# Kernel tuning notes

Measured on AMD Instinct MI355X. Metric: run time of the kernel, lower is better.

## Reference

```python
import jax, jax.numpy as jnp
import numpy as np

NUM_EMBEDDINGS = 8192
EMBEDDING_DIM = 512
BATCH = 32768
COMMITMENT_COST = 0.25
DECAY = 0.99


def setup_inputs() -> dict:
    key = jax.random.key(0)
    k1, k2, k3 = jax.random.split(key, 3)
    z = jax.random.normal(k1, (BATCH, EMBEDDING_DIM), dtype=jnp.float32)
    # codebook initialized uniform(-1/K, 1/K) as in the torch module
    codebook = jax.random.uniform(k2, (NUM_EMBEDDINGS, EMBEDDING_DIM), dtype=jnp.float32,
                                  minval=-1.0 / NUM_EMBEDDINGS, maxval=1.0 / NUM_EMBEDDINGS)
    ema_cluster_size = jnp.zeros((NUM_EMBEDDINGS,), dtype=jnp.float32)
    ema_embedding_sum = codebook.copy()
    return {"z": z, "codebook": codebook, "ema_cluster_size": ema_cluster_size,
            "ema_embedding_sum": ema_embedding_sum}


def reference(z, codebook, ema_cluster_size, ema_embedding_sum):
    K, D = codebook.shape
    B = z.shape[0]
    # squared-euclidean distances: ||z||^2 - 2 z W^T + ||W||^2  -> [B, K]
    distances = (jnp.sum(z * z, axis=1, keepdims=True)
                 - 2.0 * jnp.einsum('bd,kd->bk', z, codebook)
                 + jnp.sum(codebook * codebook, axis=1)[None, :])
    indices = jnp.argmin(distances, axis=1)            # [B]
    quantized = codebook[indices]                      # [B, D] gather

    commitment_loss = jnp.mean((z - jax.lax.stop_gradient(quantized)) ** 2)
    codebook_loss = jnp.mean((quantized - jax.lax.stop_gradient(z)) ** 2)
    vq_loss = codebook_loss + COMMITMENT_COST * commitment_loss

    # EMA statistics (training-mode buffer update, no grad)
    cluster_size = jax.ops.segment_sum(jnp.ones((B,), jnp.float32), indices, num_segments=K)
    embedding_sum = jax.ops.segment_sum(z, indices, num_segments=K)  # one-hot^T @ z
    new_ema_cluster_size = DECAY * ema_cluster_size + (1.0 - DECAY) * cluster_size
    new_ema_embedding_sum = DECAY * ema_embedding_sum + (1.0 - DECAY) * embedding_sum
    n = jnp.sum(new_ema_cluster_size)
    cs_norm = (new_ema_cluster_size + 1e-5) / (n + K * 1e-5) * n
    new_codebook = new_ema_embedding_sum / cs_norm[:, None]

    # straight-through estimator
    quantized_st = z + jax.lax.stop_gradient(quantized - z)

    # perplexity of code usage
    avg_probs = cluster_size / B
    perplexity = jnp.exp(-jnp.sum(avg_probs * jnp.log(avg_probs + 1e-10)))

    return (quantized_st, indices, commitment_loss, codebook_loss, vq_loss,
            perplexity, new_ema_cluster_size, new_ema_embedding_sum, new_codebook)
```

## Files before the change

### kernel.cpp

```cpp
#include <hip/hip_runtime.h>
#include <math.h>

typedef unsigned long long u64;
typedef unsigned int u32;
typedef unsigned short u16;
typedef __attribute__((ext_vector_type(8))) short bf16x8;
typedef __attribute__((ext_vector_type(8))) u16  u16x8;
typedef __attribute__((ext_vector_type(4))) float f32x4;

#define KC 8192
#define DD 512
#define BB 32768
#define NSPLIT 4
#define KRANGE (KC / NSPLIT)
#define BMM 128
#define BNN 128
#define NCT (KRANGE / BNN)
#define TOPS 4

#define WS_SEG   0ull
#define WS_CNT   (WS_SEG + (size_t)KC * DD * 4)
#define WS_LOSS  (WS_CNT + (size_t)KC * 4)
#define WS_W2    (WS_LOSS + 8)
#define WS_ZZ    (WS_W2 + (size_t)KC * 4)
#define WS_TI    (WS_ZZ + (size_t)BB * 4)
#define WS_CSN   (WS_TI + (size_t)NSPLIT * BB * TOPS * 4)
#define WS_WB    (WS_CSN + (size_t)KC * 4)
#define ZERO_BYTES (WS_LOSS + 8)

#define OQ  0ull
#define OI  ((size_t)BB * DD)
#define OS  (OI + BB)
#define ONC (OS + 4)
#define ONS (ONC + KC)
#define OCB (ONS + (size_t)KC * DD)

__device__ __forceinline__ u64 sortable_pack(float e, int col) {
    u32 s = __float_as_uint(e);
    s = (s & 0x80000000u) ? ~s : (s | 0x80000000u);
    return ((u64)s << 32) | (u32)col;
}
__device__ __forceinline__ u64 umin64(u64 a, u64 b) { return a < b ? a : b; }
__device__ __forceinline__ u64 umax64(u64 a, u64 b) { return a > b ? a : b; }
__device__ __forceinline__ u16 f2bf(float f) {
    u32 u = __float_as_uint(f);
    u32 r = u + 0x7FFFu + ((u >> 16) & 1u);
    return (u16)(r >> 16);
}

__global__ __launch_bounds__(256)
void cvt_kernel(const float* __restrict__ in, u16* __restrict__ out, int n8) {
    int i = blockIdx.x * 256 + threadIdx.x;
    if (i >= n8) return;
    float4 a = ((const float4*)in)[2 * i];
    float4 b = ((const float4*)in)[2 * i + 1];
    u16x8 r = { f2bf(a.x), f2bf(a.y), f2bf(a.z), f2bf(a.w),
                f2bf(b.x), f2bf(b.y), f2bf(b.z), f2bf(b.w) };
    ((u16x8*)out)[i] = r;
}

__global__ __launch_bounds__(256)
void np_sqnorm_kernel(const float* __restrict__ in, float* __restrict__ out, int rows) {
    int r = blockIdx.x * 256 + threadIdx.x;
    if (r >= rows) return;
    const float* p = in + (size_t)r * DD;
    float Bv[4];
#pragma unroll
    for (int blk = 0; blk < 4; blk++) {
        const float4* p4 = (const float4*)(p + blk * 128);
        float4 a = p4[0], b = p4[1];
        float a0 = __fmul_rn(a.x, a.x), a1 = __fmul_rn(a.y, a.y);
        float a2 = __fmul_rn(a.z, a.z), a3 = __fmul_rn(a.w, a.w);
        float a4 = __fmul_rn(b.x, b.x), a5 = __fmul_rn(b.y, b.y);
        float a6 = __fmul_rn(b.z, b.z), a7 = __fmul_rn(b.w, b.w);
#pragma unroll
        for (int t = 1; t < 16; t++) {
            a = p4[2 * t]; b = p4[2 * t + 1];
            a0 = __fadd_rn(a0, __fmul_rn(a.x, a.x)); a1 = __fadd_rn(a1, __fmul_rn(a.y, a.y));
            a2 = __fadd_rn(a2, __fmul_rn(a.z, a.z)); a3 = __fadd_rn(a3, __fmul_rn(a.w, a.w));
            a4 = __fadd_rn(a4, __fmul_rn(b.x, b.x)); a5 = __fadd_rn(a5, __fmul_rn(b.y, b.y));
            a6 = __fadd_rn(a6, __fmul_rn(b.z, b.z)); a7 = __fadd_rn(a7, __fmul_rn(b.w, b.w));
        }
        Bv[blk] = __fadd_rn(__fadd_rn(__fadd_rn(a0, a1), __fadd_rn(a2, a3)),
                            __fadd_rn(__fadd_rn(a4, a5), __fadd_rn(a6, a7)));
    }
    out[r] = __fadd_rn(__fadd_rn(Bv[0], Bv[1]), __fadd_rn(Bv[2], Bv[3]));
}

__global__ __launch_bounds__(256, 2)
void pass1_mfma_kernel(const u16* __restrict__ Zb, const u16* __restrict__ Wb,
                       const float* __restrict__ w2, int* __restrict__ ti) {
    __shared__ u64 smem64[4224];
    char* smem = (char*)smem64;

    int bx = blockIdx.x;
    int bxs = (bx & 7) * 128 + (bx >> 3);
    int sp = bxs & 3;
    int rb = bxs >> 2;
    int row0 = rb * BMM, col0 = sp * KRANGE;

    int tid = threadIdx.x;
    int lane = tid & 63, wid = tid >> 6;
    int wr = wid >> 1, wc = wid & 1;
    int l15 = lane & 15, g = lane >> 4, l7 = lane & 7;
    int srow = lane >> 3;
    int schunk = l7 ^ srow;

    u64 K3[16][3];
#pragma unroll
    for (int s = 0; s < 16; s++) { K3[s][0] = ~0ull; K3[s][1] = ~0ull; K3[s][2] = ~0ull; }

    for (int ct = 0; ct < NCT; ++ct) {
        int kc0 = col0 + ct * BNN;
        f32x4 acc[4][4];
#pragma unroll
        for (int m = 0; m < 4; m++)
#pragma unroll
            for (int n = 0; n < 4; n++) acc[m][n] = (f32x4)(0.0f);

        for (int d0 = 0; d0 < DD; d0 += 64) {
            __syncthreads();
#pragma unroll
            for (int ii = 0; ii < 4; ii++) {
                int issue = wid * 4 + ii;
                int trow = issue * 8 + srow;
                const char* gpA = (const char*)Zb +
                    (((size_t)(row0 + trow) * DD) + d0 + schunk * 8) * 2;
                __builtin_amdgcn_global_load_lds((const void*)gpA,
                    (void*)(smem + issue * 1024), 16, 0, 0);
                const char* gpB = (const char*)Wb +
                    (((size_t)(kc0 + trow) * DD) + d0 + schunk * 8) * 2;
                __builtin_amdgcn_global_load_lds((const void*)gpB,
                    (void*)(smem + 16384 + issue * 1024), 16, 0, 0);
            }
            __syncthreads();
#pragma unroll
            for (int ks = 0; ks < 2; ks++) {
                int sA = ((ks * 4 + g) ^ l7) << 4;
                bf16x8 aF[4], bF[4];
#pragma unroll
                for (int m = 0; m < 4; m++) {
                    int ar = wr * 64 + m * 16 + l15;
                    aF[m] = *(const bf16x8*)(smem + ar * 128 + sA);
                }
#pragma unroll
                for (int n = 0; n < 4; n++) {
                    int br = wc * 64 + n * 16 + l15;
                    bF[n] = *(const bf16x8*)(smem + 16384 + br * 128 + sA);
                }
#pragma unroll
                for (int m = 0; m < 4; m++)
#pragma unroll
                    for (int n = 0; n < 4; n++)
                        acc[m][n] = __builtin_amdgcn_mfma_f32_16x16x32_bf16(
                            aF[m], bF[n], acc[m][n], 0, 0, 0);
            }
        }
#pragma unroll
        for (int n = 0; n < 4; n++) {
            int col = kc0 + wc * 64 + n * 16 + l15;
            float w2c = w2[col];
#pragma unroll
            for (int m = 0; m < 4; m++) {
#pragma unroll
                for (int r = 0; r < 4; r++) {
                    float e = fmaf(-2.0f, acc[m][n][r], w2c);
                    u64 x = sortable_pack(e, col);
                    int s = m * 4 + r;
                    if (x < K3[s][2]) {
                        u64 t1 = umax64(K3[s][0], x); K3[s][0] = umin64(K3[s][0], x);
                        u64 t2 = umax64(K3[s][1], t1); K3[s][1] = umin64(K3[s][1], t1);
                        K3[s][2] = umin64(K3[s][2], t2);
                    }
                }
            }
        }
    }

    u64* mb = smem64;
    for (int ph = 0; ph < 4; ph++) {
        __syncthreads();
        if (wr == (ph >> 1)) {
            int m0 = (ph & 1) * 2;
#pragma unroll
            for (int mi = 0; mi < 2; mi++) {
#pragma unroll
                for (int r = 0; r < 4; r++) {
                    int rip = mi * 16 + g * 4 + r;
                    int slot = wc * 16 + l15;
                    int s = (m0 + mi) * 4 + r;
                    u64* dst = &mb[rip * 97 + slot * 3];
                    dst[0] = K3[s][0]; dst[1] = K3[s][1]; dst[2] = K3[s][2];
                }
            }
        }
        __syncthreads();
        if (tid < 32) {
            u64 k0 = ~0ull, k1 = ~0ull, k2 = ~0ull, k3 = ~0ull;
            for (int e2 = 0; e2 < 96; e2++) {
                u64 x = mb[tid * 97 + e2];
                if (x < k3) {
                    u64 t1 = umax64(k0, x); k0 = umin64(k0, x);
                    u64 t2 = umax64(k1, t1); k1 = umin64(k1, t1);
                    u64 t3 = umax64(k2, t2); k2 = umin64(k2, t2);
                    k3 = umin64(k3, t3);
                }
            }
            int row = row0 + ph * 32 + tid;
            size_t o = ((size_t)sp * BB + row) * TOPS;
            ti[o + 0] = (int)(u32)k0;
            ti[o + 1] = (int)(u32)k1;
            ti[o + 2] = (int)(u32)k2;
            ti[o + 3] = (int)(u32)k3;
        }
    }
}

__global__ __launch_bounds__(256)
void rerank_kernel(const float* __restrict__ Z, const float* __restrict__ W,
                   const int* __restrict__ ti, const float* __restrict__ zzv,
                   const float* __restrict__ w2,
                   float* __restrict__ outq, float* __restrict__ outi,
                   float* __restrict__ counts, float* __restrict__ seg,
                   double* __restrict__ loss_acc) {
    int row = (blockIdx.x * blockDim.x + threadIdx.x) >> 6;
    int lane = threadIdx.x & 63;
    if (row >= BB) return;
    const float* zp = Z + (size_t)row * DD;
    float zf[8];
#pragma unroll
    for (int j = 0; j < 8; j++) zf[j] = zp[lane + j * 64];
    float zz = zzv[row];

    u64 best = ~0ull;
    for (int c = 0; c < NSPLIT * TOPS; c++) {
        int ix = ti[((size_t)(c >> 2) * BB + row) * TOPS + (c & 3)];
        const float* wp = W + (size_t)ix * DD;
        double dot = 0.0;
#pragma unroll
        for (int j = 0; j < 8; j++)
            dot = fma((double)zf[j], (double)wp[lane + j * 64], dot);
#pragma unroll
        for (int o = 32; o; o >>= 1) dot += __shfl_down(dot, o, 64);
        float E = (float)dot;
        E = __shfl(E, 0, 64);
        float dist = __fadd_rn(__fadd_rn(zz, __fmul_rn(-2.0f, E)), w2[ix]);
        u64 x = sortable_pack(dist, ix);
        best = umin64(best, x);
    }
    int besti = (int)(u32)best;

    if (!lane) { outi[row] = (float)besti; atomicAdd(&counts[besti], 1.0f); }
    const float* wp = W + (size_t)besti * DD;
    double ls = 0.0;
#pragma unroll
    for (int j = 0; j < 8; j++) {
        float q = wp[lane + j * 64];
        outq[(size_t)row * DD + lane + j * 64] = __fadd_rn(zf[j], __fsub_rn(q, zf[j]));
        float d = __fsub_rn(zf[j], q);
        ls = fma((double)d, (double)d, ls);
        atomicAdd(&seg[(size_t)besti * DD + lane + j * 64], zf[j]);
    }
#pragma unroll
    for (int o = 32; o; o >>= 1) ls += __shfl_down(ls, o, 64);
    if (!lane) atomicAdd(loss_acc, ls);
}

__global__ void finalize_kernel(const float* __restrict__ ema_cs,
                                const float* __restrict__ counts,
                                const double* __restrict__ loss_acc,
                                float* __restrict__ out_ncs,
                                float* __restrict__ out_scal,
                                float* __restrict__ csnorm) {
    __shared__ double sn[256], sh[256];
    int tid = threadIdx.x;
    double nl = 0.0, hl = 0.0;
    for (int k = tid; k < KC; k += 256) {
        float c = counts[k];
        float ncs = 0.99f * ema_cs[k] + 0.01f * c;
        out_ncs[k] = ncs;
        nl += (double)ncs;
        double p = (double)c * (1.0 / (double)BB);
        hl += p * log(p + 1e-10);
    }
    sn[tid] = nl; sh[tid] = hl; __syncthreads();
    for (int s = 128; s; s >>= 1) {
        if (tid < s) { sn[tid] += sn[tid + s]; sh[tid] += sh[tid + s]; }
        __syncthreads();
    }
    if (!tid) {
        double L = loss_acc[0] * (1.0 / ((double)BB * DD));
        out_scal[0] = (float)L;
        out_scal[1] = (float)L;
        out_scal[2] = (float)(L + 0.25 * L);
        out_scal[3] = (float)exp(-sh[0]);
    }
    double n = sn[0];
    for (int k = tid; k < KC; k += 256) {
        double ncs = (double)out_ncs[k];
        csnorm[k] = (float)((ncs + 1e-5) / (n + (double)KC * 1e-5) * n);
    }
}

__global__ __launch_bounds__(256)
void ema_kernel(const float* __restrict__ ema_sum, const float* __restrict__ seg,
                const float* __restrict__ csnorm,
                float* __restrict__ out_ns, float* __restrict__ out_cb) {
    int i = blockIdx.x * 256 + threadIdx.x;
    if (i >= KC * DD / 4) return;
    int k = i >> 7;
    float4 es = ((const float4*)ema_sum)[i];
    float4 sg = ((const float4*)seg)[i];
    float4 ns;
    ns.x = 0.99f * es.x + 0.01f * sg.x;
    ns.y = 0.99f * es.y + 0.01f * sg.y;
    ns.z = 0.99f * es.z + 0.01f * sg.z;
    ns.w = 0.99f * es.w + 0.01f * sg.w;
    ((float4*)out_ns)[i] = ns;
    float cn = csnorm[k];
    float4 cb; cb.x = ns.x / cn; cb.y = ns.y / cn; cb.z = ns.z / cn; cb.w = ns.w / cn;
    ((float4*)out_cb)[i] = cb;
}

extern "C" void kernel_launch(void* const* d_in, const int* in_sizes, int n_in,
                              void* d_out, int out_size, void* d_ws, size_t ws_size,
                              hipStream_t stream) {
    (void)in_sizes; (void)n_in; (void)out_size; (void)ws_size;
    const float* Z       = (const float*)d_in[0];
    const float* W       = (const float*)d_in[1];
    const float* ema_cs  = (const float*)d_in[2];
    const float* ema_sum = (const float*)d_in[3];
    float* out = (float*)d_out;
    char* ws = (char*)d_ws;

    float*  seg  = (float*)(ws + WS_SEG);
    float*  cnt  = (float*)(ws + WS_CNT);
    double* loss = (double*)(ws + WS_LOSS);
    float*  w2   = (float*)(ws + WS_W2);
    float*  zz   = (float*)(ws + WS_ZZ);
    int*    ti   = (int*)(ws + WS_TI);
    float*  csn  = (float*)(ws + WS_CSN);
    u16*    Wb   = (u16*)(ws + WS_WB);
    u16*    Zb   = (u16*)(out + OQ);

    hipMemsetAsync(ws, 0, ZERO_BYTES, stream);
    np_sqnorm_kernel<<<KC / 256, 256, 0, stream>>>(W, w2, KC);
    np_sqnorm_kernel<<<BB / 256, 256, 0, stream>>>(Z, zz, BB);
    cvt_kernel<<<(BB * DD / 8) / 256, 256, 0, stream>>>(Z, Zb, BB * DD / 8);
    cvt_kernel<<<(KC * DD / 8) / 256, 256, 0, stream>>>(W, Wb, KC * DD / 8);
    pass1_mfma_kernel<<<(BB / BMM) * NSPLIT, 256, 0, stream>>>(Zb, Wb, w2, ti);
    rerank_kernel<<<BB / 4, 256, 0, stream>>>(Z, W, ti, zz, w2, out + OQ, out + OI, cnt, seg, loss);
    finalize_kernel<<<1, 256, 0, stream>>>(ema_cs, cnt, loss, out + ONC, out + OS, csn);
    ema_kernel<<<KC * DD / 4 / 256, 256, 0, stream>>>(ema_sum, seg, csn, out + ONS, out + OCB);
}
```

Baseline: 1.607 ms.

## Prune rerank candidates by approximate-distance margin and parallelize row norms

New measurement: 1.490 ms. -7.3%, faster.

```diff
diff --git a/kernel.cpp b/kernel.cpp
--- a/kernel.cpp
+++ b/kernel.cpp
@@ -17,6 +17,7 @@
 #define BNN 128
 #define NCT (KRANGE / BNN)
 #define TOPS 4
+#define MARGIN 6e-4f
 
 #define WS_SEG   0ull
 #define WS_CNT   (WS_SEG + (size_t)KC * DD * 4)
@@ -24,7 +25,7 @@
 #define WS_W2    (WS_LOSS + 8)
 #define WS_ZZ    (WS_W2 + (size_t)KC * 4)
 #define WS_TI    (WS_ZZ + (size_t)BB * 4)
-#define WS_CSN   (WS_TI + (size_t)NSPLIT * BB * TOPS * 4)
+#define WS_CSN   (WS_TI + (size_t)NSPLIT * BB * TOPS * 8)
 #define WS_WB    (WS_CSN + (size_t)KC * 4)
 #define ZERO_BYTES (WS_LOSS + 8)
 
@@ -39,6 +40,11 @@
     u32 s = __float_as_uint(e);
     s = (s & 0x80000000u) ? ~s : (s | 0x80000000u);
     return ((u64)s << 32) | (u32)col;
+}
+__device__ __forceinline__ float sortable_unpack_val(u64 x) {
+    u32 s = (u32)(x >> 32);
+    u32 u = (s & 0x80000000u) ? (s & 0x7fffffffu) : ~s;
+    return __uint_as_float(u);
 }
 __device__ __forceinline__ u64 umin64(u64 a, u64 b) { return a < b ? a : b; }
 __device__ __forceinline__ u64 umax64(u64 a, u64 b) { return a > b ? a : b; }
@@ -61,42 +67,33 @@
 
 __global__ __launch_bounds__(256)
 void np_sqnorm_kernel(const float* __restrict__ in, float* __restrict__ out, int rows) {
-    int r = blockIdx.x * 256 + threadIdx.x;
+    int wv = (blockIdx.x * 256 + threadIdx.x) >> 6;
+    int lane = threadIdx.x & 63;
+    int r = wv * 2 + (lane >> 5);
     if (r >= rows) return;
-    const float* p = in + (size_t)r * DD;
-    float Bv[4];
-#pragma unroll
-    for (int blk = 0; blk < 4; blk++) {
-        const float4* p4 = (const float4*)(p + blk * 128);
-        float4 a = p4[0], b = p4[1];
-        float a0 = __fmul_rn(a.x, a.x), a1 = __fmul_rn(a.y, a.y);
-        float a2 = __fmul_rn(a.z, a.z), a3 = __fmul_rn(a.w, a.w);
-        float a4 = __fmul_rn(b.x, b.x), a5 = __fmul_rn(b.y, b.y);
-        float a6 = __fmul_rn(b.z, b.z), a7 = __fmul_rn(b.w, b.w);
-#pragma unroll
-        for (int t = 1; t < 16; t++) {
-            a = p4[2 * t]; b = p4[2 * t + 1];
-            a0 = __fadd_rn(a0, __fmul_rn(a.x, a.x)); a1 = __fadd_rn(a1, __fmul_rn(a.y, a.y));
-            a2 = __fadd_rn(a2, __fmul_rn(a.z, a.z)); a3 = __fadd_rn(a3, __fmul_rn(a.w, a.w));
-            a4 = __fadd_rn(a4, __fmul_rn(b.x, b.x)); a5 = __fadd_rn(a5, __fmul_rn(b.y, b.y));
-            a6 = __fadd_rn(a6, __fmul_rn(b.z, b.z)); a7 = __fadd_rn(a7, __fmul_rn(b.w, b.w));
-        }
-        Bv[blk] = __fadd_rn(__fadd_rn(__fadd_rn(a0, a1), __fadd_rn(a2, a3)),
-                            __fadd_rn(__fadd_rn(a4, a5), __fadd_rn(a6, a7)));
-    }
-    out[r] = __fadd_rn(__fadd_rn(Bv[0], Bv[1]), __fadd_rn(Bv[2], Bv[3]));
+    int l = lane & 31, b = l >> 3, a = l & 7;
+    const float* p = in + (size_t)r * DD + b * 128 + a;
+    float s = 0.0f;
+#pragma unroll
+    for (int t = 0; t < 16; t++) { float v = p[t * 8]; s = __fadd_rn(s, __fmul_rn(v, v)); }
+    s = __fadd_rn(s, __shfl_xor(s, 1, 64));
+    s = __fadd_rn(s, __shfl_xor(s, 2, 64));
+    s = __fadd_rn(s, __shfl_xor(s, 4, 64));
+    s = __fadd_rn(s, __shfl_xor(s, 8, 64));
+    s = __fadd_rn(s, __shfl_xor(s, 16, 64));
+    if (l == 0) out[r] = s;
 }
 
 __global__ __launch_bounds__(256, 2)
 void pass1_mfma_kernel(const u16* __restrict__ Zb, const u16* __restrict__ Wb,
-                       const float* __restrict__ w2, int* __restrict__ ti) {
+                       const float* __restrict__ w2, u64* __restrict__ ti) {
     __shared__ u64 smem64[4224];
     char* smem = (char*)smem64;
 
     int bx = blockIdx.x;
-    int bxs = (bx & 7) * 128 + (bx >> 3);
-    int sp = bxs & 3;
-    int rb = bxs >> 2;
+    int xcd = bx & 7, slot = bx >> 3;
+    int sp = xcd >> 1;
+    int rb = (xcd & 1) * 128 + slot;
     int row0 = rb * BMM, col0 = sp * KRANGE;
 
     int tid = threadIdx.x;
@@ -187,9 +184,9 @@
 #pragma unroll
                 for (int r = 0; r < 4; r++) {
                     int rip = mi * 16 + g * 4 + r;
-                    int slot = wc * 16 + l15;
+                    int slot2 = wc * 16 + l15;
                     int s = (m0 + mi) * 4 + r;
-                    u64* dst = &mb[rip * 97 + slot * 3];
+                    u64* dst = &mb[rip * 97 + slot2 * 3];
                     dst[0] = K3[s][0]; dst[1] = K3[s][1]; dst[2] = K3[s][2];
                 }
             }
@@ -208,17 +205,14 @@
             }
             int row = row0 + ph * 32 + tid;
             size_t o = ((size_t)sp * BB + row) * TOPS;
-            ti[o + 0] = (int)(u32)k0;
-            ti[o + 1] = (int)(u32)k1;
-            ti[o + 2] = (int)(u32)k2;
-            ti[o + 3] = (int)(u32)k3;
+            ti[o + 0] = k0; ti[o + 1] = k1; ti[o + 2] = k2; ti[o + 3] = k3;
         }
     }
 }
 
 __global__ __launch_bounds__(256)
 void rerank_kernel(const float* __restrict__ Z, const float* __restrict__ W,
-                   const int* __restrict__ ti, const float* __restrict__ zzv,
+                   const u64* __restrict__ ti, const float* __restrict__ zzv,
                    const float* __restrict__ w2,
                    float* __restrict__ outq, float* __restrict__ outi,
                    float* __restrict__ counts, float* __restrict__ seg,
@@ -232,9 +226,21 @@
     for (int j = 0; j < 8; j++) zf[j] = zp[lane + j * 64];
     float zz = zzv[row];
 
+    u64 cand = 0;
+    if (lane < 16) cand = ti[((size_t)(lane >> 2) * BB + row) * TOPS + (lane & 3)];
+    float cv = sortable_unpack_val(cand);
+    u64 mn = (lane < 16) ? cand : ~0ull;
+#pragma unroll
+    for (int o = 32; o; o >>= 1) mn = umin64(mn, __shfl_xor(mn, o, 64));
+    float vminf = sortable_unpack_val(mn);
+    bool surv = (lane < 16) && (cv <= vminf + MARGIN);
+    unsigned long long mask = __ballot(surv);
+
     u64 best = ~0ull;
-    for (int c = 0; c < NSPLIT * TOPS; c++) {
-        int ix = ti[((size_t)(c >> 2) * BB + row) * TOPS + (c & 3)];
+    while (mask) {
+        int c = (int)(__ffsll((long long)mask) - 1); mask &= mask - 1;
+        u64 cu = __shfl(cand, c, 64);
+        int ix = (int)(u32)cu;
         const float* wp = W + (size_t)ix * DD;
         double dot = 0.0;
 #pragma unroll
@@ -245,8 +251,7 @@
         float E = (float)dot;
         E = __shfl(E, 0, 64);
         float dist = __fadd_rn(__fadd_rn(zz, __fmul_rn(-2.0f, E)), w2[ix]);
-        u64 x = sortable_pack(dist, ix);
-        best = umin64(best, x);
+        best = umin64(best, sortable_pack(dist, ix));
     }
     int besti = (int)(u32)best;
 
@@ -338,14 +343,14 @@
     double* loss = (double*)(ws + WS_LOSS);
     float*  w2   = (float*)(ws + WS_W2);
     float*  zz   = (float*)(ws + WS_ZZ);
-    int*    ti   = (int*)(ws + WS_TI);
+    u64*    ti   = (u64*)(ws + WS_TI);
     float*  csn  = (float*)(ws + WS_CSN);
     u16*    Wb   = (u16*)(ws + WS_WB);
     u16*    Zb   = (u16*)(out + OQ);
 
     hipMemsetAsync(ws, 0, ZERO_BYTES, stream);
-    np_sqnorm_kernel<<<KC / 256, 256, 0, stream>>>(W, w2, KC);
-    np_sqnorm_kernel<<<BB / 256, 256, 0, stream>>>(Z, zz, BB);
+    np_sqnorm_kernel<<<KC / 8, 256, 0, stream>>>(W, w2, KC);
+    np_sqnorm_kernel<<<BB / 8, 256, 0, stream>>>(Z, zz, BB);
     cvt_kernel<<<(BB * DD / 8) / 256, 256, 0, stream>>>(Z, Zb, BB * DD / 8);
     cvt_kernel<<<(KC * DD / 8) / 256, 256, 0, stream>>>(W, Wb, KC * DD / 8);
     pass1_mfma_kernel<<<(BB / BMM) * NSPLIT, 256, 0, stream>>>(Zb, Wb, w2, ti);
```
